# Kernel tuning notes

Hardware: AMD Instinct MI355X
Metric: run time of the kernel (lower is better)

The kernel has to match this reference:

```python
import jax, jax.numpy as jnp
import numpy as np

N_EMBED = 256
HEAD_SIZE = 64


def setup_inputs() -> dict:
    key = jax.random.key(0)
    ks = jax.random.split(key, 8)
    B, N, C, H = 4, 16384, N_EMBED, HEAD_SIZE
    inp = {
        "x0": jax.random.normal(ks[0], (B, N, C), dtype=jnp.float32),
        "x1": jax.random.normal(ks[1], (B, N, C), dtype=jnp.float32),
    }
    # torch nn.Linear weights: [out, in], y = x @ W.T (no bias, qkv_bias=False)
    scale = 1.0 / np.sqrt(C)
    names = ["Wk0", "Wk1", "Wq0", "Wq1", "Wv0", "Wv1"]
    for i, n in enumerate(names):
        inp[n] = jax.random.uniform(ks[2 + i], (H, C), dtype=jnp.float32,
                                    minval=-scale, maxval=scale)
    return inp


def reference(x0, x1, Wk0, Wk1, Wq0, Wq1, Wv0, Wv1):
    # projections: [B, N, C] @ [C, H] -> [B, N, H]
    k0 = jnp.einsum("bnc,hc->bnh", x0, Wk0)
    k1 = jnp.einsum("bnc,hc->bnh", x1, Wk1)
    q0 = jnp.einsum("bnc,hc->bnh", x0, Wq0)
    q1 = jnp.einsum("bnc,hc->bnh", x1, Wq1)
    v0 = jnp.einsum("bnc,hc->bnh", x0, Wv0)
    v1 = jnp.einsum("bnc,hc->bnh", x1, Wv1)
    # softmax over tokens (axis=-2) for keys, over head dim (-1) for queries
    k0 = jax.nn.softmax(k0, axis=-2)
    k1 = jax.nn.softmax(k1, axis=-2)
    q0 = jax.nn.softmax(q0, axis=-1)
    q1 = jax.nn.softmax(q1, axis=-1)
    # context matrices: [B, H, H]
    w0 = jnp.einsum("bnh,bnd->bhd", k0, v0)
    w1 = jnp.einsum("bnh,bnd->bhd", k1, v1)
    # cross attention outputs: [B, N, H]
    attn_x0 = jnp.einsum("bnh,bhd->bnd", q0, w1)
    attn_x1 = jnp.einsum("bnh,bhd->bnd", q1, w0)
    return (attn_x0, attn_x1)
```

## Files before the change

### kernel.cpp

```cpp
#include <hip/hip_runtime.h>


#define B_ 4
#define N_ 16384
#define C_ 256

typedef float f32x4 __attribute__((ext_vector_type(4)));
typedef __bf16 bf16x8 __attribute__((ext_vector_type(8)));
typedef unsigned short us8 __attribute__((ext_vector_type(8)));

__device__ __forceinline__ unsigned short f2bf(float f) {
  union { float f; unsigned u; } v; v.f = f;
  return (unsigned short)((v.u + 0x7FFFu + ((v.u >> 16) & 1u)) >> 16);
}
__device__ __forceinline__ float bf2f(unsigned short h) {
  union { unsigned u; float f; } v; v.u = ((unsigned)h) << 16;
  return v.f;
}

#define WPACK_OFF 0u
#define Q_OFF     262144u
#define PNW_OFF   17039360u
#define PZ_OFF    25427968u
#define WFIN_OFF  25690112u

__global__ __launch_bounds__(256) void kW_pack(
    const float* __restrict__ Wk0, const float* __restrict__ Wk1,
    const float* __restrict__ Wq0, const float* __restrict__ Wq1,
    const float* __restrict__ Wv0, const float* __restrict__ Wv1,
    unsigned short* __restrict__ wpack) {
  int t = blockIdx.x * 256 + threadIdx.x;
  int i = t & 7;
  int lane = (t >> 3) & 63;
  int q = t >> 9;
  int ks = q & 7;
  int sj = q >> 3;
  int s = sj / 12;
  int j = sj - s * 12;
  int gc = 16 * j + (lane & 15);
  int c = 32 * ks + ((lane >> 4) << 3) + i;
  int m = gc >> 6, row = gc & 63;
  const float* W;
  if (s == 0) W = (m == 0) ? Wk0 : (m == 1) ? Wq0 : Wv0;
  else        W = (m == 0) ? Wk1 : (m == 1) ? Wq1 : Wv1;
  wpack[t] = f2bf(W[row * 256 + c]);
}

__global__ __launch_bounds__(512, 2) void kA_proj(
    const float* __restrict__ x0, const float* __restrict__ x1,
    const unsigned short* __restrict__ wpack,
    unsigned short* __restrict__ qbuf, float* __restrict__ pnw,
    float* __restrict__ pz) {
  int slot = blockIdx.x;
  int bs = blockIdx.y;
  int b = bs >> 1, s = bs & 1;
  const float* x = (s ? x1 : x0) + (size_t)b * N_ * C_;
  int t = threadIdx.x;
  int w = t >> 6;
  int l = t & 63;
  int l15 = l & 15, lg = l >> 4;
  int wr = w >> 2, wc = w & 3;
  int hf = w >> 1, dp = w & 1;

  __shared__ __align__(16) char xsb[32768];
  char* pTb = xsb;
  char* vTb = xsb + 8192;
  char* qsb = xsb + 16384;

  const char* wbase = (const char*)wpack + (size_t)s * 12 * 8 * 64 * 16;

  f32x4 nwacc[2];
#pragma unroll
  for (int j2 = 0; j2 < 2; ++j2) { f32x4 z = {0.f,0.f,0.f,0.f}; nwacc[j2] = z; }
  float zacc = 0.f;

  for (int it = 0; it < 4; ++it) {
    int n0 = (slot + it * 64) * 64;

    const f32x4* xsrc = (const f32x4*)(x + (size_t)n0 * C_);
#pragma unroll 1
    for (int g2 = 0; g2 < 2; ++g2) {
#pragma unroll
      for (int i = 0; i < 4; ++i) {
        int f = t + 512 * (g2 * 4 + i);
        int row = f >> 6;
        f32x4 v = xsrc[f];
        ushort4 pk;
        pk.x = f2bf(v[0]); pk.y = f2bf(v[1]); pk.z = f2bf(v[2]); pk.w = f2bf(v[3]);
        int off = (f * 8) ^ ((row & 7) << 4);
        *(ushort4*)(xsb + off) = pk;
      }
    }
    __syncthreads();

    f32x4 acc[2][3];
#pragma unroll
    for (int rf = 0; rf < 2; ++rf)
#pragma unroll
      for (int jj = 0; jj < 3; ++jj) { f32x4 z = {0.f,0.f,0.f,0.f}; acc[rf][jj] = z; }

    bf16x8 bA[3], bB[3];
#pragma unroll
    for (int jj = 0; jj < 3; ++jj)
      bA[jj] = *(const bf16x8*)(wbase + (((size_t)((wc + 4*jj)*8 + 0))*64 + l)*16);
#pragma unroll
    for (int ks = 0; ks < 8; ++ks) {
      const bf16x8* bc = (ks & 1) ? bB : bA;
      bf16x8* bn = (ks & 1) ? bA : bB;
      if (ks < 7) {
#pragma unroll
        for (int jj = 0; jj < 3; ++jj)
          bn[jj] = *(const bf16x8*)(wbase + (((size_t)((wc + 4*jj)*8 + ks+1))*64 + l)*16);
      }
      bf16x8 a[2];
#pragma unroll
      for (int rf = 0; rf < 2; ++rf) {
        int row = (wr * 2 + rf) * 16 + l15;
        int off = (row * 512 + ks * 64 + lg * 16) ^ ((row & 7) << 4);
        a[rf] = *(const bf16x8*)(xsb + off);
      }
#pragma unroll
      for (int jj = 0; jj < 3; ++jj)
#pragma unroll
        for (int rf = 0; rf < 2; ++rf)
          acc[rf][jj] = __builtin_amdgcn_mfma_f32_16x16x32_bf16(
              a[rf], bc[jj], acc[rf][jj], 0, 0, 0);
    }
    __syncthreads();

    {
      int hcol = wc * 16 + l15;
      float zl = 0.f;
#pragma unroll
      for (int rf = 0; rf < 2; ++rf)
#pragma unroll
        for (int r = 0; r < 4; ++r) {
          float ev = __expf(acc[rf][0][r]);
          zl += ev;
          int n = (wr * 2 + rf) * 16 + lg * 4 + r;
          int off = (hcol * 128 + n * 2) ^ ((hcol & 7) << 4);
          *(unsigned short*)(pTb + off) = f2bf(ev);
        }
      zl += __shfl_xor(zl, 16);
      zl += __shfl_xor(zl, 32);
      zacc += zl;
    }
    {
#pragma unroll
      for (int rf = 0; rf < 2; ++rf)
#pragma unroll
        for (int r = 0; r < 4; ++r) {
          int n = (wr * 2 + rf) * 16 + lg * 4 + r;
          int off = (n * 128 + (wc * 16 + l15) * 2) ^ ((n & 7) << 4);
          *(unsigned short*)(qsb + off) = f2bf(acc[rf][1][r]);
        }
    }
    {
      int dcol = wc * 16 + l15;
#pragma unroll
      for (int rf = 0; rf < 2; ++rf)
#pragma unroll
        for (int r = 0; r < 4; ++r) {
          int n = (wr * 2 + rf) * 16 + lg * 4 + r;
          int off = (dcol * 128 + n * 2) ^ ((dcol & 7) << 4);
          *(unsigned short*)(vTb + off) = f2bf(acc[rf][2][r]);
        }
    }
    __syncthreads();

    {
      unsigned short* qg = qbuf + ((size_t)bs * N_ + n0) * 64;
      int n = t >> 3, c = t & 7;
      int off = (n * 128 + c * 16) ^ ((n & 7) << 4);
      us8 v = *(const us8*)(qsb + off);
      *(us8*)(qg + (size_t)t * 8) = v;
    }

#pragma unroll
    for (int k2 = 0; k2 < 2; ++k2) {
      int hh = hf * 16 + l15;
      int aoff = (hh * 128 + (k2 * 32 + lg * 8) * 2) ^ ((hh & 7) << 4);
      bf16x8 a2 = *(const bf16x8*)(pTb + aoff);
#pragma unroll
      for (int df = 0; df < 2; ++df) {
        int dd = (dp * 2 + df) * 16 + l15;
        int boff = (dd * 128 + (k2 * 32 + lg * 8) * 2) ^ ((dd & 7) << 4);
        bf16x8 b2 = *(const bf16x8*)(vTb + boff);
        nwacc[df] = __builtin_amdgcn_mfma_f32_16x16x32_bf16(a2, b2, nwacc[df], 0, 0, 0);
      }
    }
    __syncthreads();
  }

#pragma unroll
  for (int df = 0; df < 2; ++df)
#pragma unroll
    for (int r = 0; r < 4; ++r) {
      int h = hf * 16 + lg * 4 + r;
      int d = (dp * 2 + df) * 16 + l15;
      pnw[(((size_t)bs * 64 + slot) * 64 + h) * 64 + d] = nwacc[df][r];
    }
  if (lg == 0)
    pz[(((size_t)bs * 64 + slot) * 2 + wr) * 64 + wc * 16 + l15] = zacc;
}

__global__ __launch_bounds__(256) void kB_reduce(
    const float* __restrict__ pnw, const float* __restrict__ pz,
    float* __restrict__ wfin) {
  int g = blockIdx.x;
  int bs = blockIdx.y;
  int t = threadIdx.x;
  int wv = t >> 6, l = t & 63;
  __shared__ float zinv[4];
  int h = g * 4 + wv;
  float z = pz[((size_t)bs * 128 + l) * 64 + h] +
            pz[((size_t)bs * 128 + 64 + l) * 64 + h];
#pragma unroll
  for (int m = 32; m; m >>= 1) z += __shfl_xor(z, m);
  if (l == 0) zinv[wv] = 1.f / z;
  __syncthreads();
  int idx = g * 256 + t;
  float ssum = 0.f;
#pragma unroll 8
  for (int p = 0; p < 64; ++p)
    ssum += pnw[((size_t)bs * 64 + p) * 4096 + idx];
  wfin[(size_t)bs * 4096 + idx] = ssum * zinv[wv];
}

__global__ __launch_bounds__(256) void kC_out(
    const unsigned short* __restrict__ qbuf, const float* __restrict__ wfin,
    float* __restrict__ out) {
  int bs = blockIdx.y, b = bs >> 1, s = bs & 1;
  int t = threadIdx.x;
  int w = t >> 6, l = t & 63;
  int l15 = l & 15, lg = l >> 4;
  int tok0 = blockIdx.x * 64;

  __shared__ __align__(16) char cb[16384];
  char* plb = cb;
  char* wlb = cb + 8192;
  float* ob = (float*)cb;

  const float* wsrc = wfin + (size_t)(b * 2 + (1 - s)) * 4096;
#pragma unroll
  for (int rr = 0; rr < 4; ++rr) {
    int fi = t + 256 * rr;
    int h = fi >> 4, d4 = (fi & 15) * 4;
    f32x4 v = *(const f32x4*)(wsrc + h * 64 + d4);
#pragma unroll
    for (int e = 0; e < 4; ++e) {
      int d = d4 + e;
      int off = (d * 128 + h * 2) ^ ((d & 7) << 4);
      *(unsigned short*)(wlb + off) = f2bf(v[e]);
    }
  }

  {
    int tl = t >> 2, p4 = t & 3;
    const unsigned short* qr =
        qbuf + ((size_t)bs * N_ + tok0 + tl) * 64 + p4 * 16;
    us8 u0 = *(const us8*)(qr);
    us8 u1 = *(const us8*)(qr + 8);
    float e[16]; float sum = 0.f;
#pragma unroll
    for (int i = 0; i < 8; ++i) { e[i] = __expf(bf2f(u0[i])); sum += e[i]; }
#pragma unroll
    for (int i = 0; i < 8; ++i) { e[8+i] = __expf(bf2f(u1[i])); sum += e[8+i]; }
    sum += __shfl_xor(sum, 1);
    sum += __shfl_xor(sum, 2);
    float inv = 1.f / sum;
    us8 p0, p1;
#pragma unroll
    for (int i = 0; i < 8; ++i) { p0[i] = f2bf(e[i] * inv); p1[i] = f2bf(e[8+i] * inv); }
    int off = (tl * 128 + p4 * 32) ^ ((tl & 7) << 4);
    *(us8*)(plb + off) = p0;
    *(us8*)(plb + (off ^ 16)) = p1;
  }
  __syncthreads();

  f32x4 acc[4];
#pragma unroll
  for (int rf = 0; rf < 4; ++rf) { f32x4 z = {0.f,0.f,0.f,0.f}; acc[rf] = z; }
#pragma unroll
  for (int k2 = 0; k2 < 2; ++k2) {
    int dd = w * 16 + l15;
    int boff = (dd * 128 + (k2 * 32 + lg * 8) * 2) ^ ((dd & 7) << 4);
    bf16x8 bfrag = *(const bf16x8*)(wlb + boff);
#pragma unroll
    for (int rf = 0; rf < 4; ++rf) {
      int row = rf * 16 + l15;
      int aoff = (row * 128 + (k2 * 32 + lg * 8) * 2) ^ ((row & 7) << 4);
      bf16x8 afrag = *(const bf16x8*)(plb + aoff);
      acc[rf] = __builtin_amdgcn_mfma_f32_16x16x32_bf16(afrag, bfrag, acc[rf], 0, 0, 0);
    }
  }
  __syncthreads();

#pragma unroll
  for (int rf = 0; rf < 4; ++rf)
#pragma unroll
    for (int r = 0; r < 4; ++r) {
      int tok = rf * 16 + lg * 4 + r;
      int d = w * 16 + l15;
      ob[tok * 64 + d] = acc[rf][r];
    }
  __syncthreads();

  float* outp = out + (size_t)s * ((size_t)B_ * N_ * 64) +
                ((size_t)b * N_ + tok0) * 64;
#pragma unroll
  for (int r2 = 0; r2 < 4; ++r2) {
    int fi = t + 256 * r2;
    ((f32x4*)outp)[fi] = ((const f32x4*)ob)[fi];
  }
}

extern "C" void kernel_launch(void* const* d_in, const int* in_sizes, int n_in,
                              void* d_out, int out_size, void* d_ws, size_t ws_size,
                              hipStream_t stream) {
  const float* x0  = (const float*)d_in[0];
  const float* x1  = (const float*)d_in[1];
  const float* Wk0 = (const float*)d_in[2];
  const float* Wk1 = (const float*)d_in[3];
  const float* Wq0 = (const float*)d_in[4];
  const float* Wq1 = (const float*)d_in[5];
  const float* Wv0 = (const float*)d_in[6];
  const float* Wv1 = (const float*)d_in[7];
  float* out = (float*)d_out;
  char* wsb = (char*)d_ws;
  unsigned short* wpack = (unsigned short*)(wsb + WPACK_OFF);
  unsigned short* qbuf  = (unsigned short*)(wsb + Q_OFF);
  float* pnw  = (float*)(wsb + PNW_OFF);
  float* pz   = (float*)(wsb + PZ_OFF);
  float* wfin = (float*)(wsb + WFIN_OFF);

  kW_pack<<<dim3(384), dim3(256), 0, stream>>>(Wk0, Wk1, Wq0, Wq1, Wv0, Wv1, wpack);
  kA_proj<<<dim3(64, 8), dim3(512), 0, stream>>>(x0, x1, wpack, qbuf, pnw, pz);
  kB_reduce<<<dim3(16, 8), dim3(256), 0, stream>>>(pnw, pz, wfin);
  kC_out<<<dim3(256, 8), dim3(256), 0, stream>>>(qbuf, wfin, out);
}
```

Measured before the change: 61.12 us.

## Prefetch next x tile into registers during compute, drop weight double-buffer

The first x tile is loaded before the loop. Each iteration then issues global loads for the next 64-row tile into 8 float4 registers per thread before the MFMA work, and converts and writes them to shared memory after the context MFMAs, behind an extra barrier. This hides global load latency behind compute. The double-buffered weight fragment prefetch is replaced by plain per-k-step loads, likely to free registers for the prefetch buffer. The cost is higher register pressure, an extra __syncthreads per iteration, and weight load latency that is no longer hidden.

```diff
diff --git a/kernel.cpp b/kernel.cpp
--- a/kernel.cpp
+++ b/kernel.cpp
@@ -74,10 +74,8 @@
   for (int j2 = 0; j2 < 2; ++j2) { f32x4 z = {0.f,0.f,0.f,0.f}; nwacc[j2] = z; }
   float zacc = 0.f;
 
-  for (int it = 0; it < 4; ++it) {
-    int n0 = (slot + it * 64) * 64;
-
-    const f32x4* xsrc = (const f32x4*)(x + (size_t)n0 * C_);
+  {
+    const f32x4* xsrc = (const f32x4*)(x + (size_t)(slot * 64) * C_);
 #pragma unroll 1
     for (int g2 = 0; g2 < 2; ++g2) {
 #pragma unroll
@@ -91,7 +89,18 @@
         *(ushort4*)(xsb + off) = pk;
       }
     }
-    __syncthreads();
+  }
+  __syncthreads();
+
+  for (int it = 0; it < 4; ++it) {
+    int n0 = (slot + it * 64) * 64;
+
+    f32x4 pf[8];
+    if (it < 3) {
+      const f32x4* xn = (const f32x4*)(x + (size_t)((slot + (it + 1) * 64) * 64) * C_);
+#pragma unroll
+      for (int i = 0; i < 8; ++i) pf[i] = xn[t + 512 * i];
+    }
 
     f32x4 acc[2][3];
 #pragma unroll
@@ -99,19 +108,12 @@
 #pragma unroll
       for (int jj = 0; jj < 3; ++jj) { f32x4 z = {0.f,0.f,0.f,0.f}; acc[rf][jj] = z; }
 
-    bf16x8 bA[3], bB[3];
-#pragma unroll
-    for (int jj = 0; jj < 3; ++jj)
-      bA[jj] = *(const bf16x8*)(wbase + (((size_t)((wc + 4*jj)*8 + 0))*64 + l)*16);
 #pragma unroll
     for (int ks = 0; ks < 8; ++ks) {
-      const bf16x8* bc = (ks & 1) ? bB : bA;
-      bf16x8* bn = (ks & 1) ? bA : bB;
-      if (ks < 7) {
-#pragma unroll
-        for (int jj = 0; jj < 3; ++jj)
-          bn[jj] = *(const bf16x8*)(wbase + (((size_t)((wc + 4*jj)*8 + ks+1))*64 + l)*16);
-      }
+      bf16x8 bfr[3];
+#pragma unroll
+      for (int jj = 0; jj < 3; ++jj)
+        bfr[jj] = *(const bf16x8*)(wbase + (((size_t)((wc + 4*jj)*8 + ks))*64 + l)*16);
       bf16x8 a[2];
 #pragma unroll
       for (int rf = 0; rf < 2; ++rf) {
@@ -124,7 +126,7 @@
 #pragma unroll
         for (int rf = 0; rf < 2; ++rf)
           acc[rf][jj] = __builtin_amdgcn_mfma_f32_16x16x32_bf16(
-              a[rf], bc[jj], acc[rf][jj], 0, 0, 0);
+              a[rf], bfr[jj], acc[rf][jj], 0, 0, 0);
     }
     __syncthreads();
 
@@ -187,6 +189,20 @@
         int boff = (dd * 128 + (k2 * 32 + lg * 8) * 2) ^ ((dd & 7) << 4);
         bf16x8 b2 = *(const bf16x8*)(vTb + boff);
         nwacc[df] = __builtin_amdgcn_mfma_f32_16x16x32_bf16(a2, b2, nwacc[df], 0, 0, 0);
+      }
+    }
+    __syncthreads();
+
+    if (it < 3) {
+#pragma unroll
+      for (int i = 0; i < 8; ++i) {
+        int f = t + 512 * i;
+        int row = f >> 6;
+        ushort4 pk;
+        pk.x = f2bf(pf[i][0]); pk.y = f2bf(pf[i][1]);
+        pk.z = f2bf(pf[i][2]); pk.w = f2bf(pf[i][3]);
+        int off = (f * 8) ^ ((row & 7) << 4);
+        *(ushort4*)(xsb + off) = pk;
       }
     }
     __syncthreads();
```

Measured after the change: 58.78 us. 1.04x faster.
